# Kernel tuning notes

Hardware: AMD Instinct MI355X
Metric: run time of the kernel (lower is better)

The kernel has to match this reference:

```python
import jax, jax.numpy as jnp
import numpy as np
from jax import lax

B, T, V, P, L = 16, 1024, 4096, 100, 128
BLANK = 0
TEMPERATURE = 1.0


def setup_inputs() -> dict:
    key = jax.random.key(0)
    k1, k2, k3, k4, k5 = jax.random.split(key, 5)
    emissions = jax.random.normal(k1, (B, T, V), dtype=jnp.float32)
    emissions_lengths = jax.random.randint(k2, (B,), T // 2, T + 1).astype(jnp.int32)
    labels = jax.random.randint(k3, (B, L), 1, V).astype(jnp.int32)  # non-blank tokens
    labels_length = jax.random.randint(k4, (B,), L // 2, L + 1).astype(jnp.int32)
    paths = jax.random.randint(k5, (B, P, T), 0, V).astype(jnp.int32)  # sampled lattice paths
    return {"emissions": emissions, "emissions_lengths": emissions_lengths,
            "labels": labels, "labels_length": labels_length, "paths": paths}


def _edit_distance(paths, valid, labels, labels_length):
    """Levenshtein distance between each CTC-collapsed path and its reference.
    paths/valid: (B,P,T) int/bool; labels: (B,L); returns (B,P) int32."""
    refs = labels[:, None, :]                       # (B,1,L)
    js = jnp.arange(L + 1, dtype=jnp.int32)
    D0 = jnp.broadcast_to(js, (B, P, L + 1))        # D[j]=j: j insertions

    def step(D, inp):
        c, v = inp                                  # c: (B,P) token, v: (B,P) valid flag
        sub = (refs != c[..., None]).astype(jnp.int32)          # (B,P,L)
        cand_rest = jnp.minimum(D[..., 1:] + 1, D[..., :-1] + sub)
        cand = jnp.concatenate([D[..., :1] + 1, cand_rest], axis=-1)  # (B,P,L+1)
        # insertion closure: new[j] = min_{k<=j} cand[k] + (j-k), via prefix-min trick
        run = lax.associative_scan(jnp.minimum, cand - js, axis=-1)
        new = run + js
        return jnp.where(v[..., None], new, D), None

    toks = jnp.moveaxis(paths, 2, 0)                # (T,B,P)
    vals = jnp.moveaxis(valid, 2, 0)                # (T,B,P)
    D, _ = lax.scan(step, D0, (toks, vals))
    idx = jnp.broadcast_to(labels_length[:, None, None].astype(jnp.int32), (B, P, 1))
    return jnp.take_along_axis(D, idx, axis=-1)[..., 0]  # (B,P)


def reference(emissions, emissions_lengths, labels, labels_length, paths):
    logp = jax.nn.log_softmax(emissions, axis=-1)                   # (B,T,V)
    frame_mask = jnp.arange(T) < emissions_lengths[:, None]          # (B,T)
    # path total log-prob: gather logp at each path token per frame
    idx = jnp.swapaxes(paths, 1, 2)                                  # (B,T,P)
    g = jnp.take_along_axis(logp, idx, axis=2)                       # (B,T,P)
    scores = jnp.sum(g * frame_mask[:, :, None], axis=1)             # (B,P)
    posterior = jax.nn.softmax(scores / TEMPERATURE, axis=1)         # per-utterance path posterior
    # CTC collapse: drop blanks and consecutive repeats
    prev = jnp.concatenate([jnp.full((B, P, 1), -1, paths.dtype), paths[..., :-1]], axis=-1)
    valid = (paths != BLANK) & (paths != prev) & frame_mask[:, None, :]
    wers = _edit_distance(paths, valid, labels, labels_length).astype(logp.dtype)  # (B,P)
    # MWER (eq. 2): expected edit distance under path posterior, reduction='sum'
    return jnp.sum(posterior * wers)
```

## Files before the change

kernel.cpp:

```cpp
#include <hip/hip_runtime.h>
#include <stdint.h>

#define B 16
#define T 1024
#define V 4096
#define P 100
#define L 128

__global__ __launch_bounds__(256) void scores4_kernel(
    const float* __restrict__ emissions,
    const int* __restrict__ emissions_lengths,
    const int* __restrict__ paths,
    float* __restrict__ scores_part)
{
    int gid = blockIdx.x * blockDim.x + threadIdx.x;
    int wave = gid >> 6;
    int lane = threadIdx.x & 63;
    if (wave >= B * P * 4) return;
    int w  = wave & 3;
    int bp = wave >> 2;
    int b  = bp / P;
    int len = emissions_lengths[b];
    const int4* path4 = (const int4*)(paths + (size_t)bp * T);
    int4 tk = path4[w * 64 + lane];
    int tbase = 4 * (w * 64 + lane);
    const float* em = emissions + (size_t)b * T * V;

    float acc = 0.f;
    if (tbase + 0 < len) acc += em[(size_t)(tbase + 0) * V + tk.x];
    if (tbase + 1 < len) acc += em[(size_t)(tbase + 1) * V + tk.y];
    if (tbase + 2 < len) acc += em[(size_t)(tbase + 2) * V + tk.z];
    if (tbase + 3 < len) acc += em[(size_t)(tbase + 3) * V + tk.w];

    #pragma unroll
    for (int off = 32; off; off >>= 1) acc += __shfl_down(acc, off, 64);
    if (lane == 0) scores_part[bp * 4 + w] = acc;
}

__global__ __launch_bounds__(256) void wer_kernel(
    const int* __restrict__ emissions_lengths,
    const int* __restrict__ labels,
    const int* __restrict__ labels_length,
    const int* __restrict__ paths,
    float* __restrict__ wers)
{
    __shared__ unsigned short toks[4][1024];
    int gid = blockIdx.x * blockDim.x + threadIdx.x;
    int wave = gid >> 6;
    int lane = threadIdx.x & 63;
    int slot = (threadIdx.x >> 6) & 3;
    if (wave >= B * P) return;
    int b = wave / P;
    int len = emissions_lengths[b];
    int ll  = labels_length[b];
    const int* path = paths + (size_t)wave * T;

    int prev_last = -1;
    int base = 0;
    for (int t0 = 0; t0 < len; t0 += 64) {
        int c = path[t0 + lane];
        int cp = __shfl_up(c, 1, 64);
        if (lane == 0) cp = prev_last;
        bool valid = (c != 0) && (c != cp) && (t0 + lane < len);
        unsigned long long mask = __ballot(valid);
        int pos = base + __popcll(mask & ((1ull << lane) - 1ull));
        if (valid) toks[slot][pos] = (unsigned short)c;
        base += __popcll(mask);
        prev_last = __shfl(c, 63, 64);
    }
    int S = base;

    int j1 = 2 * lane + 1;
    int j2 = 2 * lane + 2;
    int r1 = labels[b * L + 2 * lane];
    int r2 = labels[b * L + 2 * lane + 1];

    int A1 = j1, B1 = j1;
    int A2 = j2, B2 = j2;
    int tok1 = 0, tok2 = 0;
    int tnext = toks[slot][(1 - 2 * lane - 2) & 1023];
    int dmax = S + ll;

    for (int d = 1; d <= dmax; d++) {
        int packed = (A2 << 16) | B2;
        int up = __shfl_up(packed, 1, 64);
        int upA, upB;
        if (lane == 0) { upA = d - 1; upB = d - 2; }
        else { upA = ((unsigned)up) >> 16; upB = up & 0xffff; }

        tok2 = tok1;
        tok1 = tnext;
        tnext = toks[slot][(d + 1 - 2 * lane - 2) & 1023];

        int t1 = d - j1;
        int n1 = min(min(A1, upA) + 1, upB + (tok1 != r1));
        if (t1 <= 0) n1 = j1;
        else if (t1 > S) n1 = A1;

        int t2 = d - j2;
        int n2 = min(min(A2, A1) + 1, B1 + (tok2 != r2));
        if (t2 <= 0) n2 = j2;
        else if (t2 > S) n2 = A2;

        B1 = A1; A1 = n1;
        B2 = A2; A2 = n2;
    }

    int va = __shfl(A1, (ll - 1) >> 1, 64);
    int vb = __shfl(A2, (ll - 2) >> 1, 64);
    int res = (ll & 1) ? va : vb;
    if (lane == 0) wers[wave] = (float)res;
}

__global__ __launch_bounds__(1024) void reduce_kernel(
    const float* __restrict__ scores_part,
    const float* __restrict__ wers,
    float* __restrict__ out)
{
    __shared__ float contrib[B];
    int lane = threadIdx.x & 63;
    int b = threadIdx.x >> 6;

    int p1 = b * P + lane;
    float s1 = scores_part[p1 * 4 + 0] + scores_part[p1 * 4 + 1]
             + scores_part[p1 * 4 + 2] + scores_part[p1 * 4 + 3];
    float w1 = wers[p1];
    bool has2 = lane < (P - 64);
    int p2 = b * P + 64 + (has2 ? lane : 0);
    float s2 = has2 ? (scores_part[p2 * 4 + 0] + scores_part[p2 * 4 + 1]
                     + scores_part[p2 * 4 + 2] + scores_part[p2 * 4 + 3])
                    : -3.4e38f;
    float w2 = has2 ? wers[p2] : 0.f;

    float m = fmaxf(s1, s2);
    #pragma unroll
    for (int off = 32; off; off >>= 1) m = fmaxf(m, __shfl_xor(m, off, 64));
    float e1 = expf(s1 - m);
    float e2 = has2 ? expf(s2 - m) : 0.f;
    float num = e1 * w1 + e2 * w2;
    float den = e1 + e2;
    #pragma unroll
    for (int off = 32; off; off >>= 1) {
        num += __shfl_xor(num, off, 64);
        den += __shfl_xor(den, off, 64);
    }
    if (lane == 0) contrib[b] = num / den;
    __syncthreads();
    if (threadIdx.x == 0) {
        float s = 0.f;
        #pragma unroll
        for (int i = 0; i < B; i++) s += contrib[i];
        out[0] = s;
    }
}

extern "C" void kernel_launch(void* const* d_in, const int* in_sizes, int n_in,
                              void* d_out, int out_size, void* d_ws, size_t ws_size,
                              hipStream_t stream) {
    const float* emissions          = (const float*)d_in[0];
    const int*   emissions_lengths  = (const int*)d_in[1];
    const int*   labels             = (const int*)d_in[2];
    const int*   labels_length      = (const int*)d_in[3];
    const int*   paths              = (const int*)d_in[4];
    float* out = (float*)d_out;

    float* scores_part = (float*)d_ws;
    float* wers        = scores_part + B * P * 4;

    scores4_kernel<<<(B * P * 4 * 64) / 256, 256, 0, stream>>>(
        emissions, emissions_lengths, paths, scores_part);
    wer_kernel<<<(B * P * 64) / 256, 256, 0, stream>>>(
        emissions_lengths, labels, labels_length, paths, wers);
    reduce_kernel<<<1, 1024, 0, stream>>>(scores_part, wers, out);
}
```

Baseline: 491.1 us.

## Replace wavefront DP edit distance with Myers bit-parallel algorithm per path

Computes each path's Levenshtein distance with Myers' bit-vector algorithm over 128-bit masks, one thread per (batch, path), using a precomputed per-batch match table (eq) built by a new kernel over the vocabulary. This replaces the anti-diagonal wavefront DP that used a whole wave per path and iterated S+L steps with shuffles. The collapse filter is folded into the step by masking updates. It adds a 1 MB table build and gathers from it, and the new grid is only 25 blocks of 64 threads, which leaves most of the GPU idle while each thread runs up to 1024 serial steps.

```diff
diff --git a/kernel.cpp b/kernel.cpp
--- a/kernel.cpp
+++ b/kernel.cpp
@@ -1,11 +1,34 @@
 #include <hip/hip_runtime.h>
 #include <stdint.h>
+
+typedef unsigned __int128 u128;
+typedef unsigned long long u64;
 
 #define B 16
 #define T 1024
 #define V 4096
 #define P 100
 #define L 128
+
+__global__ __launch_bounds__(256) void eq_build_kernel(
+    const int* __restrict__ labels,
+    const int* __restrict__ labels_length,
+    ulonglong2* __restrict__ eq)
+{
+    __shared__ int lab[L];
+    int b = blockIdx.x >> 4;
+    int c = ((blockIdx.x & 15) << 8) | threadIdx.x;
+    if (threadIdx.x < L) lab[threadIdx.x] = labels[b * L + threadIdx.x];
+    __syncthreads();
+    int ll = labels_length[b];
+    u64 lo = 0, hi = 0;
+    #pragma unroll
+    for (int j = 0; j < 64; j++) lo |= (u64)(lab[j] == c) << j;
+    #pragma unroll
+    for (int j = 0; j < 64; j++) hi |= (u64)(lab[64 + j] == c) << j;
+    if (ll < 128) hi &= (1ull << (ll - 64)) - 1ull;
+    eq[(size_t)b * V + c] = make_ulonglong2(lo, hi);
+}
 
 __global__ __launch_bounds__(256) void scores4_kernel(
     const float* __restrict__ emissions,
@@ -37,79 +60,63 @@
     if (lane == 0) scores_part[bp * 4 + w] = acc;
 }
 
-__global__ __launch_bounds__(256) void wer_kernel(
+__global__ __launch_bounds__(64) void wer_myers_kernel(
     const int* __restrict__ emissions_lengths,
-    const int* __restrict__ labels,
     const int* __restrict__ labels_length,
     const int* __restrict__ paths,
+    const ulonglong2* __restrict__ eqtab,
     float* __restrict__ wers)
 {
-    __shared__ unsigned short toks[4][1024];
-    int gid = blockIdx.x * blockDim.x + threadIdx.x;
-    int wave = gid >> 6;
-    int lane = threadIdx.x & 63;
-    int slot = (threadIdx.x >> 6) & 3;
-    if (wave >= B * P) return;
-    int b = wave / P;
+    int bp = blockIdx.x * 64 + threadIdx.x;
+    int b = bp / P;
     int len = emissions_lengths[b];
-    int ll  = labels_length[b];
-    const int* path = paths + (size_t)wave * T;
+    int ll = labels_length[b];
+    const int* path = paths + (size_t)bp * T;
+    const ulonglong2* eqb = eqtab + (size_t)b * V;
 
-    int prev_last = -1;
-    int base = 0;
-    for (int t0 = 0; t0 < len; t0 += 64) {
-        int c = path[t0 + lane];
-        int cp = __shfl_up(c, 1, 64);
-        if (lane == 0) cp = prev_last;
-        bool valid = (c != 0) && (c != cp) && (t0 + lane < len);
-        unsigned long long mask = __ballot(valid);
-        int pos = base + __popcll(mask & ((1ull << lane) - 1ull));
-        if (valid) toks[slot][pos] = (unsigned short)c;
-        base += __popcll(mask);
-        prev_last = __shfl(c, 63, 64);
+    u128 VP = (ll >= 128) ? ~(u128)0 : (((u128)1 << ll) - 1);
+    u128 VN = 0;
+    const u128 mbit = (u128)1 << (ll - 1);
+    int dist = ll;
+    int prev = -1;
+
+    auto step = [&](int c, ulonglong2 eqv, int t) {
+        bool v = (c != 0) & (c != prev) & (t < len);
+        prev = c;
+        u128 X  = ((u128)eqv.y << 64) | eqv.x;
+        u128 D0 = (((X & VP) + VP) ^ VP) | X | VN;
+        u128 HP = VN | ~(D0 | VP);
+        u128 HN = D0 & VP;
+        int delta = (int)((HP & mbit) != 0) - (int)((HN & mbit) != 0);
+        HP = (HP << 1) | 1;
+        HN = HN << 1;
+        u128 nVP = HN | ~(D0 | HP);
+        u128 nVN = HP & D0;
+        if (v) { VP = nVP; VN = nVN; dist += delta; }
+    };
+
+    int lmax = len;
+    #pragma unroll
+    for (int off = 32; off; off >>= 1) lmax = max(lmax, __shfl_xor(lmax, off, 64));
+    lmax = (lmax + 3) & ~3;
+
+    int4 tok = *(const int4*)path;
+    ulonglong2 e0 = eqb[tok.x], e1 = eqb[tok.y], e2 = eqb[tok.z], e3 = eqb[tok.w];
+
+    for (int t0 = 0; t0 < lmax; t0 += 4) {
+        int tn = min(t0 + 4, T - 4);
+        int4 ntok = *(const int4*)(path + tn);
+        ulonglong2 f0 = eqb[ntok.x], f1 = eqb[ntok.y],
+                   f2 = eqb[ntok.z], f3 = eqb[ntok.w];
+
+        step(tok.x, e0, t0 + 0);
+        step(tok.y, e1, t0 + 1);
+        step(tok.z, e2, t0 + 2);
+        step(tok.w, e3, t0 + 3);
+
+        tok = ntok; e0 = f0; e1 = f1; e2 = f2; e3 = f3;
     }
-    int S = base;
-
-    int j1 = 2 * lane + 1;
-    int j2 = 2 * lane + 2;
-    int r1 = labels[b * L + 2 * lane];
-    int r2 = labels[b * L + 2 * lane + 1];
-
-    int A1 = j1, B1 = j1;
-    int A2 = j2, B2 = j2;
-    int tok1 = 0, tok2 = 0;
-    int tnext = toks[slot][(1 - 2 * lane - 2) & 1023];
-    int dmax = S + ll;
-
-    for (int d = 1; d <= dmax; d++) {
-        int packed = (A2 << 16) | B2;
-        int up = __shfl_up(packed, 1, 64);
-        int upA, upB;
-        if (lane == 0) { upA = d - 1; upB = d - 2; }
-        else { upA = ((unsigned)up) >> 16; upB = up & 0xffff; }
-
-        tok2 = tok1;
-        tok1 = tnext;
-        tnext = toks[slot][(d + 1 - 2 * lane - 2) & 1023];
-
-        int t1 = d - j1;
-        int n1 = min(min(A1, upA) + 1, upB + (tok1 != r1));
-        if (t1 <= 0) n1 = j1;
-        else if (t1 > S) n1 = A1;
-
-        int t2 = d - j2;
-        int n2 = min(min(A2, A1) + 1, B1 + (tok2 != r2));
-        if (t2 <= 0) n2 = j2;
-        else if (t2 > S) n2 = A2;
-
-        B1 = A1; A1 = n1;
-        B2 = A2; A2 = n2;
-    }
-
-    int va = __shfl(A1, (ll - 1) >> 1, 64);
-    int vb = __shfl(A2, (ll - 2) >> 1, 64);
-    int res = (ll & 1) ? va : vb;
-    if (lane == 0) wers[wave] = (float)res;
+    wers[bp] = (float)dist;
 }
 
 __global__ __launch_bounds__(1024) void reduce_kernel(
@@ -164,12 +171,14 @@
     const int*   paths              = (const int*)d_in[4];
     float* out = (float*)d_out;
 
-    float* scores_part = (float*)d_ws;
-    float* wers        = scores_part + B * P * 4;
+    ulonglong2* eq      = (ulonglong2*)d_ws;
+    float* scores_part  = (float*)((char*)d_ws + (size_t)B * V * 16);
+    float* wers         = scores_part + B * P * 4;
 
+    eq_build_kernel<<<B * (V / 256), 256, 0, stream>>>(labels, labels_length, eq);
     scores4_kernel<<<(B * P * 4 * 64) / 256, 256, 0, stream>>>(
         emissions, emissions_lengths, paths, scores_part);
-    wer_kernel<<<(B * P * 64) / 256, 256, 0, stream>>>(
-        emissions_lengths, labels, labels_length, paths, wers);
+    wer_myers_kernel<<<B * P / 64, 64, 0, stream>>>(
+        emissions_lengths, labels_length, paths, eq, wers);
     reduce_kernel<<<1, 1024, 0, stream>>>(scores_part, wers, out);
 }
```

Result: slower. 564.4 us (+14.9%).
